# Kernel tuning notes

Measured on AMD Instinct MI355X. Metric: run time of the kernel, lower is better.

The kernel has to match this reference:

```python
import jax, jax.numpy as jnp
from jax import lax
import numpy as np
import math

NUM_CLASSES = 81
N_PER_IMG = 1024
NUM_IMAGES = 8
SCORE_THRESH = 0.05
NMS_THRESH = 0.5
DETS_PER_IMG = 100
WX, WY, WW, WH = 10.0, 10.0, 5.0, 5.0
BBOX_XFORM_CLIP = math.log(1000.0 / 16.0)


def setup_inputs() -> dict:
    key = jax.random.key(0)
    k1, k2, k3, k4 = jax.random.split(key, 4)
    M = NUM_IMAGES * N_PER_IMG
    H, W = 800, 1333
    class_logits = jax.random.normal(k1, (M, NUM_CLASSES), dtype=jnp.float32) * 3.0
    box_regression = jax.random.normal(k2, (M, 4 * NUM_CLASSES), dtype=jnp.float32) * 0.5
    # valid xyxy proposals inside the image
    xy1 = jax.random.uniform(k3, (M, 2), dtype=jnp.float32) * jnp.array([W * 0.7, H * 0.7], jnp.float32)
    wh = jax.random.uniform(k4, (M, 2), dtype=jnp.float32) * jnp.array([W * 0.3, H * 0.3], jnp.float32) + 4.0
    proposals = jnp.concatenate([xy1, xy1 + wh], axis=1)
    return {"class_logits": class_logits, "box_regression": box_regression,
            "proposals": proposals, "height": H, "width": W}


def _decode(rel_codes, boxes):
    widths = boxes[:, 2] - boxes[:, 0] + 1.0
    heights = boxes[:, 3] - boxes[:, 1] + 1.0
    ctr_x = boxes[:, 0] + 0.5 * widths
    ctr_y = boxes[:, 1] + 0.5 * heights
    rel = rel_codes.reshape(rel_codes.shape[0], -1, 4)  # [M, C, 4]
    dx = rel[:, :, 0] / WX
    dy = rel[:, :, 1] / WY
    dw = jnp.minimum(rel[:, :, 2] / WW, BBOX_XFORM_CLIP)
    dh = jnp.minimum(rel[:, :, 3] / WH, BBOX_XFORM_CLIP)
    pctr_x = dx * widths[:, None] + ctr_x[:, None]
    pctr_y = dy * heights[:, None] + ctr_y[:, None]
    pw = jnp.exp(dw) * widths[:, None]
    ph = jnp.exp(dh) * heights[:, None]
    return jnp.stack([pctr_x - 0.5 * pw, pctr_y - 0.5 * ph,
                      pctr_x + 0.5 * pw - 1.0, pctr_y + 0.5 * ph - 1.0], axis=-1)


def _clip(boxes, height, width):
    # boxes [..., 4] xyxy, clamp to [0, W-1] x [0, H-1]
    x = jnp.clip(boxes[..., 0::2], 0.0, float(width - 1))
    y = jnp.clip(boxes[..., 1::2], 0.0, float(height - 1))
    return jnp.stack([x[..., 0], y[..., 0], x[..., 1], y[..., 1]], axis=-1)


def _iou_matrix(b):
    x1, y1, x2, y2 = b[:, 0], b[:, 1], b[:, 2], b[:, 3]
    area = (x2 - x1 + 1.0) * (y2 - y1 + 1.0)
    xx1 = jnp.maximum(x1[:, None], x1[None, :])
    yy1 = jnp.maximum(y1[:, None], y1[None, :])
    xx2 = jnp.minimum(x2[:, None], x2[None, :])
    yy2 = jnp.minimum(y2[:, None], y2[None, :])
    inter = jnp.clip(xx2 - xx1 + 1.0, 0.0) * jnp.clip(yy2 - yy1 + 1.0, 0.0)
    return inter / (area[:, None] + area[None, :] - inter)


def _per_class(scores_j, boxes_j):
    # scores_j [N], boxes_j [N,4] -> sorted scores/boxes + greedy-NMS keep mask
    N = scores_j.shape[0]
    valid = scores_j > SCORE_THRESH
    s = jnp.where(valid, scores_j, 0.0)  # softmax scores are > 0
    order = jnp.argsort(-s)
    s_sorted = s[order]
    b_sorted = boxes_j[order]
    valid_sorted = valid[order]
    iou = _iou_matrix(b_sorted)  # [N, N]
    idxs = jnp.arange(N)

    def body(i, keep):
        sup = (iou[i] > NMS_THRESH) & keep[i] & (idxs > i)
        return keep & ~sup

    keep = lax.fori_loop(0, N, body, valid_sorted)
    return s_sorted, b_sorted, keep


def _per_image(prob_i, boxes_i):
    # prob_i [N, C], boxes_i [N, C, 4]; skip background class 0
    C = prob_i.shape[1]
    fg_scores = prob_i[:, 1:].T                      # [C-1, N]
    fg_boxes = jnp.swapaxes(boxes_i[:, 1:, :], 0, 1)  # [C-1, N, 4]
    s_sorted, b_sorted, keep = jax.vmap(_per_class)(fg_scores, fg_boxes)
    labels = jnp.broadcast_to(jnp.arange(1, C, dtype=jnp.int32)[:, None], s_sorted.shape)
    flat_s = jnp.where(keep, s_sorted, 0.0).reshape(-1)
    vals, idx = lax.top_k(flat_s, DETS_PER_IMG)      # detections-per-image limit
    boxes_out = b_sorted.reshape(-1, 4)[idx]
    labels_out = labels.reshape(-1)[idx]
    ok = vals > SCORE_THRESH
    return (jnp.where(ok, vals, 0.0),
            jnp.where(ok[:, None], boxes_out, 0.0),
            jnp.where(ok, labels_out, 0))


def reference(class_logits, box_regression, proposals, height, width):
    prob = jax.nn.softmax(class_logits, axis=-1)          # [M, C]
    dec = _decode(box_regression, proposals)              # [M, C, 4]
    dec = _clip(dec, height, width)
    B, N, C = NUM_IMAGES, N_PER_IMG, NUM_CLASSES
    prob = prob.reshape(B, N, C)
    dec = dec.reshape(B, N, C, 4)
    scores, boxes, labels = lax.map(lambda a: _per_image(a[0], a[1]), (prob, dec))
    return scores, boxes, labels
```

## Files before the change

### kernel.cpp

```cpp
#include <hip/hip_runtime.h>
#include <stdint.h>
#include <math.h>

#define NCLS 81
#define NFG  80
#define NPI  1024
#define NIMG 8
#define DETS 100
#define SCORE_T 0.05f
#define NMS_T   0.5f
#define NCAND   (NFG * DETS)
#define CAND_CAP 2048
#define FASTN 256
#define ROWS 64

static constexpr float BBOX_CLIP = 4.1351665567423557f;

__global__ __launch_bounds__(256) void softmax_probT(
    const float* __restrict__ logits, float* __restrict__ probT, int M)
{
    __shared__ float tile[ROWS * NCLS];
    __shared__ float mx[ROWS], dn[ROWS];
    int t = threadIdx.x;
    int rbase = blockIdx.x * ROWS;

    for (int idx = t; idx < ROWS * NCLS; idx += 256)
        tile[idx] = logits[(size_t)rbase * NCLS + idx];
    __syncthreads();

    if (t < ROWS) {
        const float* r = tile + t * NCLS;
        float m = r[0];
        #pragma unroll
        for (int j = 1; j < NCLS; ++j) m = fmaxf(m, r[j]);
        float s = 0.f;
        #pragma unroll
        for (int j = 0; j < NCLS; ++j) s += expf(r[j] - m);
        mx[t] = m; dn[t] = s;
    }
    __syncthreads();

    for (int o = t; o < ROWS * NFG; o += 256) {
        int r = o & 63;
        int c = o >> 6;
        float v = expf(tile[r * NCLS + (c + 1)] - mx[r]) / dn[r];
        probT[(size_t)c * M + rbase + r] = v;
    }
}

__global__ __launch_bounds__(256) void per_class_nms(
    const float* __restrict__ probT, const float* __restrict__ boxreg,
    const float* __restrict__ props, const int* __restrict__ hptr,
    const int* __restrict__ wptr, int* __restrict__ out_cnt,
    float* __restrict__ out_score, unsigned* __restrict__ out_key,
    float* __restrict__ out_box, int M)
{
    int pid = blockIdx.x;
    int img = pid / NFG;
    int c   = pid % NFG;
    int cls = c + 1;

    __shared__ float box_lds[NPI][4];
    __shared__ unsigned long long key[NPI];
    __shared__ int keep[NPI];
    __shared__ float sbox[FASTN][4];
    __shared__ float sarea[FASTN];
    __shared__ unsigned long long mask[FASTN][FASTN/64];
    __shared__ unsigned long long keepw[FASTN/64];
    __shared__ unsigned wpre[4];
    __shared__ int cnt;

    int t = threadIdx.x;
    float W1 = (float)(*wptr - 1);
    float H1 = (float)(*hptr - 1);

    if (t == 0) cnt = 0;
    for (int i = t; i < NPI; i += 256) key[i] = 0ULL;
    __syncthreads();

    {
        const float4 pv = *(const float4*)(probT + (size_t)c * M + img * NPI + 4 * t);
        float pr[4] = {pv.x, pv.y, pv.z, pv.w};
        #pragma unroll
        for (int j = 0; j < 4; ++j) {
            if (pr[j] > SCORE_T) {
                int m = 4 * t + j;
                int g = img * NPI + m;
                const float4 pb = *(const float4*)(props + (size_t)g * 4);
                float x1 = pb.x, y1 = pb.y, x2 = pb.z, y2 = pb.w;
                float w  = x2 - x1 + 1.0f, h = y2 - y1 + 1.0f;
                float cx = x1 + 0.5f * w,  cy = y1 + 0.5f * h;
                const float4 rc = *(const float4*)(boxreg + (size_t)g * (4 * NCLS) + 4 * cls);
                float dx = rc.x / 10.0f, dy = rc.y / 10.0f;
                float dw = fminf(rc.z / 5.0f, BBOX_CLIP);
                float dh = fminf(rc.w / 5.0f, BBOX_CLIP);
                float pcx = dx * w + cx, pcy = dy * h + cy;
                float pw = expf(dw) * w, ph = expf(dh) * h;
                float bx1 = pcx - 0.5f * pw;
                float by1 = pcy - 0.5f * ph;
                float bx2 = pcx + 0.5f * pw - 1.0f;
                float by2 = pcy + 0.5f * ph - 1.0f;
                bx1 = fminf(fmaxf(bx1, 0.f), W1);
                bx2 = fminf(fmaxf(bx2, 0.f), W1);
                by1 = fminf(fmaxf(by1, 0.f), H1);
                by2 = fminf(fmaxf(by2, 0.f), H1);
                box_lds[m][0] = bx1; box_lds[m][1] = by1;
                box_lds[m][2] = bx2; box_lds[m][3] = by2;
                int p = atomicAdd(&cnt, 1);
                unsigned fb = __float_as_uint(pr[j]);
                key[p] = ((unsigned long long)fb << 32) | (unsigned)(NPI - 1 - m);
            }
        }
    }
    __syncthreads();
    int n = cnt;

    if (n <= 64) {
        if (t < 64) {
            int lane = t;
            unsigned long long k = (lane < n) ? key[lane] : 0ULL;
            #pragma unroll
            for (int kk = 2; kk <= 64; kk <<= 1) {
                #pragma unroll
                for (int j = kk >> 1; j > 0; j >>= 1) {
                    unsigned long long o = __shfl_xor(k, j, 64);
                    bool up = ((lane & kk) == 0);
                    bool lower = ((lane & j) == 0);
                    bool take_max = (up == lower);
                    k = take_max ? (k > o ? k : o) : (k < o ? k : o);
                }
            }
            bool valid = (lane < n);
            float bx1 = 0.f, by1 = 0.f, bx2 = 0.f, by2 = 0.f, area = 0.f;
            if (valid) {
                int mi = NPI - 1 - (int)(k & 0xFFFFFFFFu);
                bx1 = box_lds[mi][0]; by1 = box_lds[mi][1];
                bx2 = box_lds[mi][2]; by2 = box_lds[mi][3];
                area = (bx2 - bx1 + 1.f) * (by2 - by1 + 1.f);
            }
            unsigned long long sup = 0ULL;
            for (int i = 0; i < n; ++i) {
                bool alive = !((sup >> i) & 1ULL);
                float ax1 = __shfl(bx1, i, 64), ay1 = __shfl(by1, i, 64);
                float ax2 = __shfl(bx2, i, 64), ay2 = __shfl(by2, i, 64);
                float aarea = __shfl(area, i, 64);
                bool s = false;
                if (alive && valid && lane > i) {
                    float xx1 = fmaxf(ax1, bx1), yy1 = fmaxf(ay1, by1);
                    float xx2 = fminf(ax2, bx2), yy2 = fminf(ay2, by2);
                    float iw = fmaxf(xx2 - xx1 + 1.f, 0.f);
                    float ih = fmaxf(yy2 - yy1 + 1.f, 0.f);
                    float inter = iw * ih;
                    float iou = inter / (aarea + area - inter);
                    s = iou > NMS_T;
                }
                sup |= __ballot(s);
            }
            bool kept = valid && !((sup >> lane) & 1ULL);
            unsigned long long keptm = __ballot(kept);
            int rank = __popcll(keptm & ((1ULL << lane) - 1ULL));
            if (kept && rank < DETS) {
                int slot = pid * DETS + rank;
                out_score[slot] = __uint_as_float((unsigned)(k >> 32));
                out_key[slot] = (unsigned)(c * NPI + lane);
                out_box[slot * 4 + 0] = bx1;
                out_box[slot * 4 + 1] = by1;
                out_box[slot * 4 + 2] = bx2;
                out_box[slot * 4 + 3] = by2;
            }
            if (lane == 0) {
                int tot = __popcll(keptm);
                out_cnt[pid] = tot < DETS ? tot : DETS;
            }
        }
        return;
    }

    int P = 2;
    while (P < n) P <<= 1;
    for (int k = 2; k <= P; k <<= 1) {
        for (int j = k >> 1; j > 0; j >>= 1) {
            for (int i = t; i < P; i += 256) {
                int ixj = i ^ j;
                if (ixj > i) {
                    unsigned long long a = key[i], b = key[ixj];
                    bool up = (i & k) == 0;
                    if (up ? (a < b) : (a > b)) { key[i] = b; key[ixj] = a; }
                }
            }
            __syncthreads();
        }
    }

    for (int i = t; i < NPI; i += 256) keep[i] = 0;
    __syncthreads();

    if (n <= FASTN) {
        for (int i = t; i < n; i += 256) {
            int mi = NPI - 1 - (int)(key[i] & 0xFFFFFFFFu);
            float bx1 = box_lds[mi][0], by1 = box_lds[mi][1];
            float bx2 = box_lds[mi][2], by2 = box_lds[mi][3];
            sbox[i][0] = bx1; sbox[i][1] = by1; sbox[i][2] = bx2; sbox[i][3] = by2;
            sarea[i] = (bx2 - bx1 + 1.f) * (by2 - by1 + 1.f);
        }
        __syncthreads();
        int nwords = ((n + 63) >> 6);
        for (int w = t; w < n * (FASTN/64); w += 256) {
            int i = w >> 2, wb = w & 3;
            if (wb >= nwords || ((wb + 1) << 6) - 1 <= i) { mask[i][wb] = 0ULL; continue; }
            float ax1 = sbox[i][0], ay1 = sbox[i][1];
            float ax2 = sbox[i][2], ay2 = sbox[i][3];
            float aarea = sarea[i];
            unsigned long long bits = 0ULL;
            int jbase = wb << 6;
            #pragma unroll 4
            for (int b = 0; b < 64; ++b) {
                int j = jbase + b;
                if (j < n && j > i) {
                    float bx1 = sbox[j][0], by1 = sbox[j][1];
                    float bx2 = sbox[j][2], by2 = sbox[j][3];
                    float xx1 = fmaxf(ax1, bx1), yy1 = fmaxf(ay1, by1);
                    float xx2 = fminf(ax2, bx2), yy2 = fminf(ay2, by2);
                    float iw = fmaxf(xx2 - xx1 + 1.f, 0.f);
                    float ih = fmaxf(yy2 - yy1 + 1.f, 0.f);
                    float inter = iw * ih;
                    float iou = inter / (aarea + sarea[j] - inter);
                    if (iou > NMS_T) bits |= (1ULL << b);
                }
            }
            mask[i][wb] = bits;
        }
        __syncthreads();
        if (t < 64) {
            int lane = t;
            unsigned long long kb = 0ULL;
            if (lane < 4) {
                int rem = n - (lane << 6);
                if (rem >= 64) kb = ~0ULL;
                else if (rem > 0) kb = (1ULL << rem) - 1ULL;
            }
            unsigned long long rm = 0ULL;
            for (int i = 0; i < n; ++i) {
                unsigned long long rw = __shfl(rm, i >> 6, 64);
                if (!((rw >> (i & 63)) & 1ULL)) {
                    unsigned long long mrow = (lane < 4) ? mask[i][lane] : 0ULL;
                    rm |= mrow;
                }
            }
            if (lane < 4) keepw[lane] = kb & ~rm;
        }
        __syncthreads();
        for (int i = t; i < n; i += 256)
            keep[i] = (int)((keepw[i >> 6] >> (i & 63)) & 1ULL);
        __syncthreads();
    } else {
        for (int i = t; i < n; i += 256) keep[i] = 1;
        __syncthreads();
        for (int i = 0; i < n; ++i) {
            if (keep[i]) {
                unsigned long long ki = key[i];
                int mi = NPI - 1 - (int)(ki & 0xFFFFFFFFu);
                float ax1 = box_lds[mi][0], ay1 = box_lds[mi][1];
                float ax2 = box_lds[mi][2], ay2 = box_lds[mi][3];
                float aarea = (ax2 - ax1 + 1.f) * (ay2 - ay1 + 1.f);
                for (int jj = i + 1 + t; jj < n; jj += 256) {
                    if (keep[jj]) {
                        int mj = NPI - 1 - (int)(key[jj] & 0xFFFFFFFFu);
                        float bx1 = box_lds[mj][0], by1 = box_lds[mj][1];
                        float bx2 = box_lds[mj][2], by2 = box_lds[mj][3];
                        float xx1 = fmaxf(ax1, bx1), yy1 = fmaxf(ay1, by1);
                        float xx2 = fminf(ax2, bx2), yy2 = fminf(ay2, by2);
                        float iw = fmaxf(xx2 - xx1 + 1.f, 0.f);
                        float ih = fmaxf(yy2 - yy1 + 1.f, 0.f);
                        float inter = iw * ih;
                        float barea = (bx2 - bx1 + 1.f) * (by2 - by1 + 1.f);
                        float iou = inter / (aarea + barea - inter);
                        if (iou > NMS_T) keep[jj] = 0;
                    }
                }
            }
            __syncthreads();
        }
    }

    {
        int lane = t & 63, w = t >> 6;
        int k0 = keep[4 * t], k1 = keep[4 * t + 1];
        int k2 = keep[4 * t + 2], k3 = keep[4 * t + 3];
        unsigned s = (unsigned)(k0 + k1 + k2 + k3);
        unsigned v = s;
        #pragma unroll
        for (int off = 1; off < 64; off <<= 1) {
            unsigned u = __shfl_up(v, off, 64);
            v += (lane >= off) ? u : 0u;
        }
        if (lane == 63) wpre[w] = v;
        __syncthreads();
        unsigned woff = 0;
        for (int w2 = 0; w2 < w; ++w2) woff += wpre[w2];
        unsigned before = v + woff - s;
        unsigned r = before;
        #pragma unroll
        for (int j = 0; j < 4; ++j) {
            int i = 4 * t + j;
            int kv = (j == 0) ? k0 : (j == 1) ? k1 : (j == 2) ? k2 : k3;
            if (kv && r < DETS) {
                unsigned long long ki = key[i];
                int mi = NPI - 1 - (int)(ki & 0xFFFFFFFFu);
                int slot = pid * DETS + (int)r;
                out_score[slot] = __uint_as_float((unsigned)(ki >> 32));
                out_key[slot] = (unsigned)(c * NPI + i);
                out_box[slot * 4 + 0] = box_lds[mi][0];
                out_box[slot * 4 + 1] = box_lds[mi][1];
                out_box[slot * 4 + 2] = box_lds[mi][2];
                out_box[slot * 4 + 3] = box_lds[mi][3];
            }
            r += (unsigned)kv;
        }
        __syncthreads();
        if (t == 0) {
            unsigned tot = wpre[0] + wpre[1] + wpre[2] + wpre[3];
            out_cnt[pid] = (int)(tot < DETS ? tot : DETS);
        }
    }
}

__device__ __forceinline__ void suffix_select(
    unsigned* hist, unsigned* wtot, int K, int* outB, unsigned* outAbove)
{
    int t = threadIdx.x, lane = t & 63, w = t >> 6;
    unsigned c0 = hist[4 * t], c1 = hist[4 * t + 1];
    unsigned c2 = hist[4 * t + 2], c3 = hist[4 * t + 3];
    unsigned ps = c0 + c1 + c2 + c3;
    unsigned v = ps;
    #pragma unroll
    for (int off = 1; off < 64; off <<= 1) {
        unsigned u = __shfl_down(v, off, 64);
        v += (lane + off < 64) ? u : 0u;
    }
    if (lane == 0) wtot[w] = v;
    __syncthreads();
    unsigned woff = 0;
    for (int w2 = w + 1; w2 < 16; ++w2) woff += wtot[w2];
    unsigned Sown = v + woff;
    unsigned A3 = Sown - ps;
    unsigned A2 = A3 + c3, A1 = A2 + c2, A0 = A1 + c1;
    unsigned A[4] = {A0, A1, A2, A3};
    unsigned C[4] = {c0, c1, c2, c3};
    #pragma unroll
    for (int j = 0; j < 4; ++j) {
        if ((int)A[j] < K && (int)(A[j] + C[j]) >= K) {
            *outB = 4 * t + j;
            *outAbove = A[j];
        }
    }
    __syncthreads();
}

__global__ __launch_bounds__(1024) void topk_merge(
    const int* __restrict__ cnts, const float* __restrict__ escore,
    const unsigned* __restrict__ ekey, const float* __restrict__ ebox,
    float* __restrict__ out)
{
    int img = blockIdx.x;
    __shared__ unsigned sc[NCAND];
    __shared__ unsigned hist[4096];
    __shared__ unsigned long long cand[CAND_CAP];
    __shared__ unsigned wtot[16];
    __shared__ int sB1, sB2, sNc;
    __shared__ unsigned sAb1, sAb2;

    int t = threadIdx.x;
    if (t == 0) { sB1 = 0; sB2 = 0; sNc = 0; sAb1 = 0; sAb2 = 0; }
    for (int p = t; p < NCAND; p += 1024) {
        int cc = p / DETS, k = p % DETS;
        unsigned fb = 0;
        if (k < cnts[img * NFG + cc]) fb = __float_as_uint(escore[img * NCAND + p]);
        sc[p] = fb;
    }
    for (int i = t; i < 4096; i += 1024) hist[i] = 0;
    __syncthreads();

    for (int p = t; p < NCAND; p += 1024) {
        unsigned fb = sc[p];
        if (fb) atomicAdd(&hist[fb >> 19], 1u);
    }
    __syncthreads();
    suffix_select(hist, wtot, DETS, &sB1, &sAb1);
    int B1 = sB1;
    unsigned ab1 = sAb1;

    for (int i = t; i < 4096; i += 1024) hist[i] = 0;
    __syncthreads();
    for (int p = t; p < NCAND; p += 1024) {
        unsigned fb = sc[p];
        if (fb && (int)(fb >> 19) == B1) atomicAdd(&hist[(fb >> 7) & 0xFFFu], 1u);
    }
    __syncthreads();
    suffix_select(hist, wtot, DETS - (int)ab1, &sB2, &sAb2);
    int B2 = sB2;

    for (int p = t; p < NCAND; p += 1024) {
        unsigned fb = sc[p];
        if (fb) {
            int d1 = (int)(fb >> 19);
            bool ok = d1 > B1 || (d1 == B1 && (int)((fb >> 7) & 0xFFFu) >= B2);
            if (ok) {
                int pos = atomicAdd(&sNc, 1);
                if (pos < CAND_CAP) {
                    unsigned fk = ekey[img * NCAND + p];
                    unsigned low = ((0x1FFFFu - fk) << 13) | (unsigned)p;
                    cand[pos] = ((unsigned long long)fb << 32) | low;
                }
            }
        }
    }
    __syncthreads();
    int nc = sNc < CAND_CAP ? sNc : CAND_CAP;
    int P = 128;
    while (P < nc) P <<= 1;
    for (int i = t; i < P; i += 1024)
        if (i >= nc) cand[i] = 0ULL;
    __syncthreads();

    for (int k = 2; k <= P; k <<= 1) {
        for (int j = k >> 1; j > 0; j >>= 1) {
            for (int i = t; i < P; i += 1024) {
                int ixj = i ^ j;
                if (ixj > i) {
                    unsigned long long a = cand[i], b = cand[ixj];
                    bool up = (i & k) == 0;
                    if (up ? (a < b) : (a > b)) { cand[i] = b; cand[ixj] = a; }
                }
            }
            __syncthreads();
        }
    }

    float* oScore = out;
    float* oBox   = out + NIMG * DETS;
    float* oLab   = out + NIMG * DETS * 5;

    if (t < DETS) {
        unsigned long long b = cand[t];
        int o = img * DETS + t;
        if (b != 0ULL) {
            float scv = __uint_as_float((unsigned)(b >> 32));
            unsigned low = (unsigned)(b & 0xFFFFFFFFu);
            unsigned flatkey = 0x1FFFFu - ((low >> 13) & 0x1FFFFu);
            int p = (int)(low & 0x1FFFu);
            int gp = img * NCAND + p;
            oScore[o] = scv;
            oBox[o * 4 + 0] = ebox[gp * 4 + 0];
            oBox[o * 4 + 1] = ebox[gp * 4 + 1];
            oBox[o * 4 + 2] = ebox[gp * 4 + 2];
            oBox[o * 4 + 3] = ebox[gp * 4 + 3];
            oLab[o] = (float)((flatkey >> 10) + 1);
        } else {
            oScore[o] = 0.f;
            oBox[o * 4 + 0] = 0.f; oBox[o * 4 + 1] = 0.f;
            oBox[o * 4 + 2] = 0.f; oBox[o * 4 + 3] = 0.f;
            oLab[o] = 0.f;
        }
    }
}

extern "C" void kernel_launch(void* const* d_in, const int* in_sizes, int n_in,
                              void* d_out, int out_size, void* d_ws, size_t ws_size,
                              hipStream_t stream) {
    const float* logits = (const float*)d_in[0];
    const float* boxreg = (const float*)d_in[1];
    const float* props  = (const float*)d_in[2];
    const int*   hptr   = (const int*)d_in[3];
    const int*   wptr   = (const int*)d_in[4];
    float* out = (float*)d_out;
    int M = in_sizes[0] / NCLS;

    char* ws = (char*)d_ws;
    float*    probT  = (float*)ws;    ws += (size_t)NFG * M * sizeof(float);
    int*      cnt    = (int*)ws;      ws += (size_t)NIMG * NFG * sizeof(int);
    float*    escore = (float*)ws;    ws += (size_t)NIMG * NCAND * sizeof(float);
    unsigned* ekey   = (unsigned*)ws; ws += (size_t)NIMG * NCAND * sizeof(unsigned);
    float*    ebox   = (float*)ws;    ws += (size_t)NIMG * NCAND * 4 * sizeof(float);

    softmax_probT<<<M / ROWS, 256, 0, stream>>>(logits, probT, M);
    per_class_nms<<<NIMG * NFG, 256, 0, stream>>>(
        probT, boxreg, props, hptr, wptr, cnt, escore, ekey, ebox, M);
    topk_merge<<<NIMG, 1024, 0, stream>>>(cnt, escore, ekey, ebox, out);
}
```

Before: 61.07 us.

## Fuse softmax, per-class NMS and top-k merge into one cooperative kernel

Replaces the three kernel launches with a single cooperative kernel of 512 blocks that runs softmax, per-class NMS (grid-strided over 640 image/class pairs) and the per-image top-k merge, with grid-wide syncs between the stages. Stage shared memory is overlaid through a union. The merge now uses 256 threads and reads scores straight from global memory instead of staging them in LDS. The aim is to remove launch gaps, at the cost of grid.sync overhead and fewer resident blocks during NMS. A fallback runs the old three-kernel path if the cooperative launch fails.

```diff
diff --git a/kernel.cpp b/kernel.cpp
--- a/kernel.cpp
+++ b/kernel.cpp
@@ -1,6 +1,9 @@
 #include <hip/hip_runtime.h>
+#include <hip/hip_cooperative_groups.h>
 #include <stdint.h>
 #include <math.h>
+
+namespace cg = cooperative_groups;
 
 #define NCLS 81
 #define NFG  80
@@ -13,8 +16,454 @@
 #define CAND_CAP 2048
 #define FASTN 256
 #define ROWS 64
+#define GRID_BLOCKS 512
 
 static constexpr float BBOX_CLIP = 4.1351665567423557f;
+
+struct ShP1 {
+    float tile[ROWS * NCLS];
+    float mx[ROWS], dn[ROWS];
+};
+struct ShP2 {
+    float box[NPI][4];
+    unsigned long long key[NPI];
+    int keep[NPI];
+    float sbox[FASTN][4];
+    float sarea[FASTN];
+    unsigned long long mask[FASTN][FASTN/64];
+    unsigned long long keepw[FASTN/64];
+    unsigned wpre[4];
+};
+struct ShP3 {
+    unsigned hist[4096];
+    unsigned long long cand[CAND_CAP];
+    int cnts[NFG];
+    unsigned wtot[4];
+    int B1, B2, Nc;
+    unsigned Ab1, Ab2;
+};
+union ShU { ShP1 p1; ShP2 p2; ShP3 p3; };
+
+__device__ __forceinline__ void suffix_select256(
+    unsigned* hist, unsigned* wtot, int K, int* outB, unsigned* outAbove)
+{
+    int t = threadIdx.x, lane = t & 63, w = t >> 6;
+    unsigned loc[16]; unsigned ps = 0;
+    #pragma unroll
+    for (int j = 0; j < 16; ++j) { loc[j] = hist[t * 16 + j]; ps += loc[j]; }
+    unsigned v = ps;
+    #pragma unroll
+    for (int off = 1; off < 64; off <<= 1) {
+        unsigned u = __shfl_down(v, off, 64);
+        v += (lane + off < 64) ? u : 0u;
+    }
+    if (lane == 0) wtot[w] = v;
+    __syncthreads();
+    unsigned woff = 0;
+    for (int w2 = w + 1; w2 < 4; ++w2) woff += wtot[w2];
+    unsigned base = v + woff - ps;
+    unsigned suf = 0;
+    #pragma unroll
+    for (int j = 15; j >= 0; --j) {
+        unsigned A = base + suf;
+        if ((int)A < K && (int)(A + loc[j]) >= K) { *outB = t * 16 + j; *outAbove = A; }
+        suf += loc[j];
+    }
+    __syncthreads();
+}
+
+__global__ __launch_bounds__(256, 2) void fpn_fused(
+    const float* __restrict__ logits, const float* __restrict__ boxreg,
+    const float* __restrict__ props, const int* __restrict__ hptr,
+    const int* __restrict__ wptr, float* __restrict__ probT,
+    int* __restrict__ gcnt, float* __restrict__ escore,
+    unsigned* __restrict__ ekey, float* __restrict__ ebox,
+    float* __restrict__ out, int M)
+{
+    cg::grid_group grid = cg::this_grid();
+    __shared__ ShU sh;
+    __shared__ int cnt;
+    int t = threadIdx.x;
+    int bid = blockIdx.x;
+
+    if (bid < M / ROWS) {
+        int rbase = bid * ROWS;
+        for (int idx = t; idx < ROWS * NCLS; idx += 256)
+            sh.p1.tile[idx] = logits[(size_t)rbase * NCLS + idx];
+        __syncthreads();
+        if (t < ROWS) {
+            const float* r = sh.p1.tile + t * NCLS;
+            float m = r[0];
+            #pragma unroll
+            for (int j = 1; j < NCLS; ++j) m = fmaxf(m, r[j]);
+            float s = 0.f;
+            #pragma unroll
+            for (int j = 0; j < NCLS; ++j) s += expf(r[j] - m);
+            sh.p1.mx[t] = m; sh.p1.dn[t] = s;
+        }
+        __syncthreads();
+        for (int o = t; o < ROWS * NFG; o += 256) {
+            int r = o & 63;
+            int c = o >> 6;
+            float v = expf(sh.p1.tile[r * NCLS + (c + 1)] - sh.p1.mx[r]) / sh.p1.dn[r];
+            probT[(size_t)c * M + rbase + r] = v;
+        }
+    }
+    grid.sync();
+
+    for (int pid = bid; pid < NIMG * NFG; pid += GRID_BLOCKS) {
+        int img = pid / NFG;
+        int c   = pid % NFG;
+        int cls = c + 1;
+        float W1 = (float)(*wptr - 1);
+        float H1 = (float)(*hptr - 1);
+
+        if (t == 0) cnt = 0;
+        for (int i = t; i < NPI; i += 256) sh.p2.key[i] = 0ULL;
+        __syncthreads();
+
+        {
+            const float4 pv = *(const float4*)(probT + (size_t)c * M + img * NPI + 4 * t);
+            float pr[4] = {pv.x, pv.y, pv.z, pv.w};
+            #pragma unroll
+            for (int j = 0; j < 4; ++j) {
+                if (pr[j] > SCORE_T) {
+                    int m = 4 * t + j;
+                    int g = img * NPI + m;
+                    const float4 pb = *(const float4*)(props + (size_t)g * 4);
+                    float x1 = pb.x, y1 = pb.y, x2 = pb.z, y2 = pb.w;
+                    float w  = x2 - x1 + 1.0f, h = y2 - y1 + 1.0f;
+                    float cx = x1 + 0.5f * w,  cy = y1 + 0.5f * h;
+                    const float4 rc = *(const float4*)(boxreg + (size_t)g * (4 * NCLS) + 4 * cls);
+                    float dx = rc.x / 10.0f, dy = rc.y / 10.0f;
+                    float dw = fminf(rc.z / 5.0f, BBOX_CLIP);
+                    float dh = fminf(rc.w / 5.0f, BBOX_CLIP);
+                    float pcx = dx * w + cx, pcy = dy * h + cy;
+                    float pw = expf(dw) * w, ph = expf(dh) * h;
+                    float bx1 = pcx - 0.5f * pw;
+                    float by1 = pcy - 0.5f * ph;
+                    float bx2 = pcx + 0.5f * pw - 1.0f;
+                    float by2 = pcy + 0.5f * ph - 1.0f;
+                    bx1 = fminf(fmaxf(bx1, 0.f), W1);
+                    bx2 = fminf(fmaxf(bx2, 0.f), W1);
+                    by1 = fminf(fmaxf(by1, 0.f), H1);
+                    by2 = fminf(fmaxf(by2, 0.f), H1);
+                    sh.p2.box[m][0] = bx1; sh.p2.box[m][1] = by1;
+                    sh.p2.box[m][2] = bx2; sh.p2.box[m][3] = by2;
+                    int p = atomicAdd(&cnt, 1);
+                    unsigned fb = __float_as_uint(pr[j]);
+                    sh.p2.key[p] = ((unsigned long long)fb << 32) | (unsigned)(NPI - 1 - m);
+                }
+            }
+        }
+        __syncthreads();
+        int n = cnt;
+
+        if (n <= 64) {
+            if (t < 64) {
+                int lane = t;
+                unsigned long long k = (lane < n) ? sh.p2.key[lane] : 0ULL;
+                #pragma unroll
+                for (int kk = 2; kk <= 64; kk <<= 1) {
+                    #pragma unroll
+                    for (int j = kk >> 1; j > 0; j >>= 1) {
+                        unsigned long long o = __shfl_xor(k, j, 64);
+                        bool up = ((lane & kk) == 0);
+                        bool lower = ((lane & j) == 0);
+                        bool take_max = (up == lower);
+                        k = take_max ? (k > o ? k : o) : (k < o ? k : o);
+                    }
+                }
+                bool valid = (lane < n);
+                float bx1 = 0.f, by1 = 0.f, bx2 = 0.f, by2 = 0.f, area = 0.f;
+                if (valid) {
+                    int mi = NPI - 1 - (int)(k & 0xFFFFFFFFu);
+                    bx1 = sh.p2.box[mi][0]; by1 = sh.p2.box[mi][1];
+                    bx2 = sh.p2.box[mi][2]; by2 = sh.p2.box[mi][3];
+                    area = (bx2 - bx1 + 1.f) * (by2 - by1 + 1.f);
+                }
+                unsigned long long sup = 0ULL;
+                for (int i = 0; i < n; ++i) {
+                    bool alive = !((sup >> i) & 1ULL);
+                    float ax1 = __shfl(bx1, i, 64), ay1 = __shfl(by1, i, 64);
+                    float ax2 = __shfl(bx2, i, 64), ay2 = __shfl(by2, i, 64);
+                    float aarea = __shfl(area, i, 64);
+                    bool s = false;
+                    if (alive && valid && lane > i) {
+                        float xx1 = fmaxf(ax1, bx1), yy1 = fmaxf(ay1, by1);
+                        float xx2 = fminf(ax2, bx2), yy2 = fminf(ay2, by2);
+                        float iw = fmaxf(xx2 - xx1 + 1.f, 0.f);
+                        float ih = fmaxf(yy2 - yy1 + 1.f, 0.f);
+                        float inter = iw * ih;
+                        float iou = inter / (aarea + area - inter);
+                        s = iou > NMS_T;
+                    }
+                    sup |= __ballot(s);
+                }
+                bool kept = valid && !((sup >> lane) & 1ULL);
+                unsigned long long keptm = __ballot(kept);
+                int rank = __popcll(keptm & ((1ULL << lane) - 1ULL));
+                if (kept && rank < DETS) {
+                    int slot = pid * DETS + rank;
+                    escore[slot] = __uint_as_float((unsigned)(k >> 32));
+                    ekey[slot] = (unsigned)(c * NPI + lane);
+                    ebox[slot * 4 + 0] = bx1;
+                    ebox[slot * 4 + 1] = by1;
+                    ebox[slot * 4 + 2] = bx2;
+                    ebox[slot * 4 + 3] = by2;
+                }
+                if (lane == 0) {
+                    int tot = __popcll(keptm);
+                    gcnt[pid] = tot < DETS ? tot : DETS;
+                }
+            }
+        } else {
+            int P = 2;
+            while (P < n) P <<= 1;
+            for (int k = 2; k <= P; k <<= 1) {
+                for (int j = k >> 1; j > 0; j >>= 1) {
+                    for (int i = t; i < P; i += 256) {
+                        int ixj = i ^ j;
+                        if (ixj > i) {
+                            unsigned long long a = sh.p2.key[i], b = sh.p2.key[ixj];
+                            bool up = (i & k) == 0;
+                            if (up ? (a < b) : (a > b)) { sh.p2.key[i] = b; sh.p2.key[ixj] = a; }
+                        }
+                    }
+                    __syncthreads();
+                }
+            }
+
+            for (int i = t; i < NPI; i += 256) sh.p2.keep[i] = 0;
+            __syncthreads();
+
+            if (n <= FASTN) {
+                for (int i = t; i < n; i += 256) {
+                    int mi = NPI - 1 - (int)(sh.p2.key[i] & 0xFFFFFFFFu);
+                    float bx1 = sh.p2.box[mi][0], by1 = sh.p2.box[mi][1];
+                    float bx2 = sh.p2.box[mi][2], by2 = sh.p2.box[mi][3];
+                    sh.p2.sbox[i][0] = bx1; sh.p2.sbox[i][1] = by1;
+                    sh.p2.sbox[i][2] = bx2; sh.p2.sbox[i][3] = by2;
+                    sh.p2.sarea[i] = (bx2 - bx1 + 1.f) * (by2 - by1 + 1.f);
+                }
+                __syncthreads();
+                int nwords = ((n + 63) >> 6);
+                for (int w = t; w < n * (FASTN/64); w += 256) {
+                    int i = w >> 2, wb = w & 3;
+                    if (wb >= nwords || ((wb + 1) << 6) - 1 <= i) { sh.p2.mask[i][wb] = 0ULL; continue; }
+                    float ax1 = sh.p2.sbox[i][0], ay1 = sh.p2.sbox[i][1];
+                    float ax2 = sh.p2.sbox[i][2], ay2 = sh.p2.sbox[i][3];
+                    float aarea = sh.p2.sarea[i];
+                    unsigned long long bits = 0ULL;
+                    int jbase = wb << 6;
+                    #pragma unroll 4
+                    for (int b = 0; b < 64; ++b) {
+                        int j = jbase + b;
+                        if (j < n && j > i) {
+                            float bx1 = sh.p2.sbox[j][0], by1 = sh.p2.sbox[j][1];
+                            float bx2 = sh.p2.sbox[j][2], by2 = sh.p2.sbox[j][3];
+                            float xx1 = fmaxf(ax1, bx1), yy1 = fmaxf(ay1, by1);
+                            float xx2 = fminf(ax2, bx2), yy2 = fminf(ay2, by2);
+                            float iw = fmaxf(xx2 - xx1 + 1.f, 0.f);
+                            float ih = fmaxf(yy2 - yy1 + 1.f, 0.f);
+                            float inter = iw * ih;
+                            float iou = inter / (aarea + sh.p2.sarea[j] - inter);
+                            if (iou > NMS_T) bits |= (1ULL << b);
+                        }
+                    }
+                    sh.p2.mask[i][wb] = bits;
+                }
+                __syncthreads();
+                if (t < 64) {
+                    int lane = t;
+                    unsigned long long kb = 0ULL;
+                    if (lane < 4) {
+                        int rem = n - (lane << 6);
+                        if (rem >= 64) kb = ~0ULL;
+                        else if (rem > 0) kb = (1ULL << rem) - 1ULL;
+                    }
+                    unsigned long long rm = 0ULL;
+                    for (int i = 0; i < n; ++i) {
+                        unsigned long long rw = __shfl(rm, i >> 6, 64);
+                        if (!((rw >> (i & 63)) & 1ULL)) {
+                            unsigned long long mrow = (lane < 4) ? sh.p2.mask[i][lane] : 0ULL;
+                            rm |= mrow;
+                        }
+                    }
+                    if (lane < 4) sh.p2.keepw[lane] = kb & ~rm;
+                }
+                __syncthreads();
+                for (int i = t; i < n; i += 256)
+                    sh.p2.keep[i] = (int)((sh.p2.keepw[i >> 6] >> (i & 63)) & 1ULL);
+                __syncthreads();
+            } else {
+                for (int i = t; i < n; i += 256) sh.p2.keep[i] = 1;
+                __syncthreads();
+                for (int i = 0; i < n; ++i) {
+                    if (sh.p2.keep[i]) {
+                        unsigned long long ki = sh.p2.key[i];
+                        int mi = NPI - 1 - (int)(ki & 0xFFFFFFFFu);
+                        float ax1 = sh.p2.box[mi][0], ay1 = sh.p2.box[mi][1];
+                        float ax2 = sh.p2.box[mi][2], ay2 = sh.p2.box[mi][3];
+                        float aarea = (ax2 - ax1 + 1.f) * (ay2 - ay1 + 1.f);
+                        for (int jj = i + 1 + t; jj < n; jj += 256) {
+                            if (sh.p2.keep[jj]) {
+                                int mj = NPI - 1 - (int)(sh.p2.key[jj] & 0xFFFFFFFFu);
+                                float bx1 = sh.p2.box[mj][0], by1 = sh.p2.box[mj][1];
+                                float bx2 = sh.p2.box[mj][2], by2 = sh.p2.box[mj][3];
+                                float xx1 = fmaxf(ax1, bx1), yy1 = fmaxf(ay1, by1);
+                                float xx2 = fminf(ax2, bx2), yy2 = fminf(ay2, by2);
+                                float iw = fmaxf(xx2 - xx1 + 1.f, 0.f);
+                                float ih = fmaxf(yy2 - yy1 + 1.f, 0.f);
+                                float inter = iw * ih;
+                                float barea = (bx2 - bx1 + 1.f) * (by2 - by1 + 1.f);
+                                float iou = inter / (aarea + barea - inter);
+                                if (iou > NMS_T) sh.p2.keep[jj] = 0;
+                            }
+                        }
+                    }
+                    __syncthreads();
+                }
+            }
+
+            {
+                int lane = t & 63, w = t >> 6;
+                int k0 = sh.p2.keep[4 * t], k1 = sh.p2.keep[4 * t + 1];
+                int k2 = sh.p2.keep[4 * t + 2], k3 = sh.p2.keep[4 * t + 3];
+                unsigned s = (unsigned)(k0 + k1 + k2 + k3);
+                unsigned v = s;
+                #pragma unroll
+                for (int off = 1; off < 64; off <<= 1) {
+                    unsigned u = __shfl_up(v, off, 64);
+                    v += (lane >= off) ? u : 0u;
+                }
+                if (lane == 63) sh.p2.wpre[w] = v;
+                __syncthreads();
+                unsigned woff = 0;
+                for (int w2 = 0; w2 < w; ++w2) woff += sh.p2.wpre[w2];
+                unsigned r = v + woff - s;
+                #pragma unroll
+                for (int j = 0; j < 4; ++j) {
+                    int i = 4 * t + j;
+                    int kv = (j == 0) ? k0 : (j == 1) ? k1 : (j == 2) ? k2 : k3;
+                    if (kv && r < DETS) {
+                        unsigned long long ki = sh.p2.key[i];
+                        int mi = NPI - 1 - (int)(ki & 0xFFFFFFFFu);
+                        int slot = pid * DETS + (int)r;
+                        escore[slot] = __uint_as_float((unsigned)(ki >> 32));
+                        ekey[slot] = (unsigned)(c * NPI + i);
+                        ebox[slot * 4 + 0] = sh.p2.box[mi][0];
+                        ebox[slot * 4 + 1] = sh.p2.box[mi][1];
+                        ebox[slot * 4 + 2] = sh.p2.box[mi][2];
+                        ebox[slot * 4 + 3] = sh.p2.box[mi][3];
+                    }
+                    r += (unsigned)kv;
+                }
+                __syncthreads();
+                if (t == 0) {
+                    unsigned tot = sh.p2.wpre[0] + sh.p2.wpre[1] + sh.p2.wpre[2] + sh.p2.wpre[3];
+                    gcnt[pid] = (int)(tot < DETS ? tot : DETS);
+                }
+            }
+        }
+        __syncthreads();
+    }
+    grid.sync();
+
+    if (bid < NIMG) {
+        int img = bid;
+        if (t < NFG) sh.p3.cnts[t] = gcnt[img * NFG + t];
+        if (t == 0) { sh.p3.B1 = 0; sh.p3.B2 = 0; sh.p3.Nc = 0; sh.p3.Ab1 = 0; sh.p3.Ab2 = 0; }
+        for (int i = t; i < 4096; i += 256) sh.p3.hist[i] = 0;
+        __syncthreads();
+
+        for (int p = t; p < NCAND; p += 256) {
+            if ((p % DETS) < sh.p3.cnts[p / DETS]) {
+                unsigned fb = __float_as_uint(escore[img * NCAND + p]);
+                atomicAdd(&sh.p3.hist[fb >> 19], 1u);
+            }
+        }
+        __syncthreads();
+        suffix_select256(sh.p3.hist, sh.p3.wtot, DETS, &sh.p3.B1, &sh.p3.Ab1);
+        int B1 = sh.p3.B1; unsigned ab1 = sh.p3.Ab1;
+
+        for (int i = t; i < 4096; i += 256) sh.p3.hist[i] = 0;
+        __syncthreads();
+        for (int p = t; p < NCAND; p += 256) {
+            if ((p % DETS) < sh.p3.cnts[p / DETS]) {
+                unsigned fb = __float_as_uint(escore[img * NCAND + p]);
+                if ((int)(fb >> 19) == B1) atomicAdd(&sh.p3.hist[(fb >> 7) & 0xFFFu], 1u);
+            }
+        }
+        __syncthreads();
+        suffix_select256(sh.p3.hist, sh.p3.wtot, DETS - (int)ab1, &sh.p3.B2, &sh.p3.Ab2);
+        int B2 = sh.p3.B2;
+
+        for (int p = t; p < NCAND; p += 256) {
+            if ((p % DETS) < sh.p3.cnts[p / DETS]) {
+                unsigned fb = __float_as_uint(escore[img * NCAND + p]);
+                int d1 = (int)(fb >> 19);
+                bool ok = d1 > B1 || (d1 == B1 && (int)((fb >> 7) & 0xFFFu) >= B2);
+                if (ok) {
+                    int pos = atomicAdd(&sh.p3.Nc, 1);
+                    if (pos < CAND_CAP) {
+                        unsigned fk = ekey[img * NCAND + p];
+                        sh.p3.cand[pos] = ((unsigned long long)fb << 32)
+                                        | (((0x1FFFFu - fk) << 13) | (unsigned)p);
+                    }
+                }
+            }
+        }
+        __syncthreads();
+        int nc = sh.p3.Nc < CAND_CAP ? sh.p3.Nc : CAND_CAP;
+        int P = 128;
+        while (P < nc) P <<= 1;
+        for (int i = t; i < P; i += 256)
+            if (i >= nc) sh.p3.cand[i] = 0ULL;
+        __syncthreads();
+
+        for (int k = 2; k <= P; k <<= 1) {
+            for (int j = k >> 1; j > 0; j >>= 1) {
+                for (int i = t; i < P; i += 256) {
+                    int ixj = i ^ j;
+                    if (ixj > i) {
+                        unsigned long long a = sh.p3.cand[i], b = sh.p3.cand[ixj];
+                        bool up = (i & k) == 0;
+                        if (up ? (a < b) : (a > b)) { sh.p3.cand[i] = b; sh.p3.cand[ixj] = a; }
+                    }
+                }
+                __syncthreads();
+            }
+        }
+
+        float* oScore = out;
+        float* oBox   = out + NIMG * DETS;
+        float* oLab   = out + NIMG * DETS * 5;
+
+        if (t < DETS) {
+            unsigned long long b = sh.p3.cand[t];
+            int o = img * DETS + t;
+            if (b != 0ULL) {
+                float scv = __uint_as_float((unsigned)(b >> 32));
+                unsigned low = (unsigned)(b & 0xFFFFFFFFu);
+                unsigned flatkey = 0x1FFFFu - ((low >> 13) & 0x1FFFFu);
+                int p = (int)(low & 0x1FFFu);
+                int gp = img * NCAND + p;
+                oScore[o] = scv;
+                oBox[o * 4 + 0] = ebox[gp * 4 + 0];
+                oBox[o * 4 + 1] = ebox[gp * 4 + 1];
+                oBox[o * 4 + 2] = ebox[gp * 4 + 2];
+                oBox[o * 4 + 3] = ebox[gp * 4 + 3];
+                oLab[o] = (float)((flatkey >> 10) + 1);
+            } else {
+                oScore[o] = 0.f;
+                oBox[o * 4 + 0] = 0.f; oBox[o * 4 + 1] = 0.f;
+                oBox[o * 4 + 2] = 0.f; oBox[o * 4 + 3] = 0.f;
+                oLab[o] = 0.f;
+            }
+        }
+    }
+}
 
 __global__ __launch_bounds__(256) void softmax_probT(
     const float* __restrict__ logits, float* __restrict__ probT, int M)
@@ -23,11 +472,9 @@
     __shared__ float mx[ROWS], dn[ROWS];
     int t = threadIdx.x;
     int rbase = blockIdx.x * ROWS;
-
     for (int idx = t; idx < ROWS * NCLS; idx += 256)
         tile[idx] = logits[(size_t)rbase * NCLS + idx];
     __syncthreads();
-
     if (t < ROWS) {
         const float* r = tile + t * NCLS;
         float m = r[0];
@@ -39,12 +486,10 @@
         mx[t] = m; dn[t] = s;
     }
     __syncthreads();
-
     for (int o = t; o < ROWS * NFG; o += 256) {
         int r = o & 63;
         int c = o >> 6;
-        float v = expf(tile[r * NCLS + (c + 1)] - mx[r]) / dn[r];
-        probT[(size_t)c * M + rbase + r] = v;
+        probT[(size_t)c * M + rbase + r] = expf(tile[r * NCLS + (c + 1)] - mx[r]) / dn[r];
     }
 }
 
@@ -59,25 +504,15 @@
     int img = pid / NFG;
     int c   = pid % NFG;
     int cls = c + 1;
-
-    __shared__ float box_lds[NPI][4];
-    __shared__ unsigned long long key[NPI];
-    __shared__ int keep[NPI];
-    __shared__ float sbox[FASTN][4];
-    __shared__ float sarea[FASTN];
-    __shared__ unsigned long long mask[FASTN][FASTN/64];
-    __shared__ unsigned long long keepw[FASTN/64];
-    __shared__ unsigned wpre[4];
+    __shared__ ShP2 sp;
     __shared__ int cnt;
-
     int t = threadIdx.x;
     float W1 = (float)(*wptr - 1);
     float H1 = (float)(*hptr - 1);
 
     if (t == 0) cnt = 0;
-    for (int i = t; i < NPI; i += 256) key[i] = 0ULL;
-    __syncthreads();
-
+    for (int i = t; i < NPI; i += 256) sp.key[i] = 0ULL;
+    __syncthreads();
     {
         const float4 pv = *(const float4*)(probT + (size_t)c * M + img * NPI + 4 * t);
         float pr[4] = {pv.x, pv.y, pv.z, pv.w};
@@ -96,19 +531,15 @@
                 float dh = fminf(rc.w / 5.0f, BBOX_CLIP);
                 float pcx = dx * w + cx, pcy = dy * h + cy;
                 float pw = expf(dw) * w, ph = expf(dh) * h;
-                float bx1 = pcx - 0.5f * pw;
-                float by1 = pcy - 0.5f * ph;
-                float bx2 = pcx + 0.5f * pw - 1.0f;
-                float by2 = pcy + 0.5f * ph - 1.0f;
-                bx1 = fminf(fmaxf(bx1, 0.f), W1);
-                bx2 = fminf(fmaxf(bx2, 0.f), W1);
-                by1 = fminf(fmaxf(by1, 0.f), H1);
-                by2 = fminf(fmaxf(by2, 0.f), H1);
-                box_lds[m][0] = bx1; box_lds[m][1] = by1;
-                box_lds[m][2] = bx2; box_lds[m][3] = by2;
+                float bx1 = fminf(fmaxf(pcx - 0.5f * pw, 0.f), W1);
+                float by1 = fminf(fmaxf(pcy - 0.5f * ph, 0.f), H1);
+                float bx2 = fminf(fmaxf(pcx + 0.5f * pw - 1.0f, 0.f), W1);
+                float by2 = fminf(fmaxf(pcy + 0.5f * ph - 1.0f, 0.f), H1);
+                sp.box[m][0] = bx1; sp.box[m][1] = by1;
+                sp.box[m][2] = bx2; sp.box[m][3] = by2;
                 int p = atomicAdd(&cnt, 1);
-                unsigned fb = __float_as_uint(pr[j]);
-                key[p] = ((unsigned long long)fb << 32) | (unsigned)(NPI - 1 - m);
+                sp.key[p] = ((unsigned long long)__float_as_uint(pr[j]) << 32)
+                          | (unsigned)(NPI - 1 - m);
             }
         }
     }
@@ -118,15 +549,13 @@
     if (n <= 64) {
         if (t < 64) {
             int lane = t;
-            unsigned long long k = (lane < n) ? key[lane] : 0ULL;
+            unsigned long long k = (lane < n) ? sp.key[lane] : 0ULL;
             #pragma unroll
             for (int kk = 2; kk <= 64; kk <<= 1) {
                 #pragma unroll
                 for (int j = kk >> 1; j > 0; j >>= 1) {
                     unsigned long long o = __shfl_xor(k, j, 64);
-                    bool up = ((lane & kk) == 0);
-                    bool lower = ((lane & j) == 0);
-                    bool take_max = (up == lower);
+                    bool take_max = (((lane & kk) == 0) == ((lane & j) == 0));
                     k = take_max ? (k > o ? k : o) : (k < o ? k : o);
                 }
             }
@@ -134,8 +563,8 @@
             float bx1 = 0.f, by1 = 0.f, bx2 = 0.f, by2 = 0.f, area = 0.f;
             if (valid) {
                 int mi = NPI - 1 - (int)(k & 0xFFFFFFFFu);
-                bx1 = box_lds[mi][0]; by1 = box_lds[mi][1];
-                bx2 = box_lds[mi][2]; by2 = box_lds[mi][3];
+                bx1 = sp.box[mi][0]; by1 = sp.box[mi][1];
+                bx2 = sp.box[mi][2]; by2 = sp.box[mi][3];
                 area = (bx2 - bx1 + 1.f) * (by2 - by1 + 1.f);
             }
             unsigned long long sup = 0ULL;
@@ -151,8 +580,7 @@
                     float iw = fmaxf(xx2 - xx1 + 1.f, 0.f);
                     float ih = fmaxf(yy2 - yy1 + 1.f, 0.f);
                     float inter = iw * ih;
-                    float iou = inter / (aarea + area - inter);
-                    s = iou > NMS_T;
+                    s = inter / (aarea + area - inter) > NMS_T;
                 }
                 sup |= __ballot(s);
             }
@@ -163,10 +591,8 @@
                 int slot = pid * DETS + rank;
                 out_score[slot] = __uint_as_float((unsigned)(k >> 32));
                 out_key[slot] = (unsigned)(c * NPI + lane);
-                out_box[slot * 4 + 0] = bx1;
-                out_box[slot * 4 + 1] = by1;
-                out_box[slot * 4 + 2] = bx2;
-                out_box[slot * 4 + 3] = by2;
+                out_box[slot * 4 + 0] = bx1; out_box[slot * 4 + 1] = by1;
+                out_box[slot * 4 + 2] = bx2; out_box[slot * 4 + 3] = by2;
             }
             if (lane == 0) {
                 int tot = __popcll(keptm);
@@ -183,52 +609,51 @@
             for (int i = t; i < P; i += 256) {
                 int ixj = i ^ j;
                 if (ixj > i) {
-                    unsigned long long a = key[i], b = key[ixj];
+                    unsigned long long a = sp.key[i], b = sp.key[ixj];
                     bool up = (i & k) == 0;
-                    if (up ? (a < b) : (a > b)) { key[i] = b; key[ixj] = a; }
+                    if (up ? (a < b) : (a > b)) { sp.key[i] = b; sp.key[ixj] = a; }
                 }
             }
             __syncthreads();
         }
     }
-
-    for (int i = t; i < NPI; i += 256) keep[i] = 0;
+    for (int i = t; i < NPI; i += 256) sp.keep[i] = 0;
     __syncthreads();
 
     if (n <= FASTN) {
         for (int i = t; i < n; i += 256) {
-            int mi = NPI - 1 - (int)(key[i] & 0xFFFFFFFFu);
-            float bx1 = box_lds[mi][0], by1 = box_lds[mi][1];
-            float bx2 = box_lds[mi][2], by2 = box_lds[mi][3];
-            sbox[i][0] = bx1; sbox[i][1] = by1; sbox[i][2] = bx2; sbox[i][3] = by2;
-            sarea[i] = (bx2 - bx1 + 1.f) * (by2 - by1 + 1.f);
+            int mi = NPI - 1 - (int)(sp.key[i] & 0xFFFFFFFFu);
+            float bx1 = sp.box[mi][0], by1 = sp.box[mi][1];
+            float bx2 = sp.box[mi][2], by2 = sp.box[mi][3];
+            sp.sbox[i][0] = bx1; sp.sbox[i][1] = by1;
+            sp.sbox[i][2] = bx2; sp.sbox[i][3] = by2;
+            sp.sarea[i] = (bx2 - bx1 + 1.f) * (by2 - by1 + 1.f);
         }
         __syncthreads();
         int nwords = ((n + 63) >> 6);
         for (int w = t; w < n * (FASTN/64); w += 256) {
             int i = w >> 2, wb = w & 3;
-            if (wb >= nwords || ((wb + 1) << 6) - 1 <= i) { mask[i][wb] = 0ULL; continue; }
-            float ax1 = sbox[i][0], ay1 = sbox[i][1];
-            float ax2 = sbox[i][2], ay2 = sbox[i][3];
-            float aarea = sarea[i];
+            if (wb >= nwords || ((wb + 1) << 6) - 1 <= i) { sp.mask[i][wb] = 0ULL; continue; }
+            float ax1 = sp.sbox[i][0], ay1 = sp.sbox[i][1];
+            float ax2 = sp.sbox[i][2], ay2 = sp.sbox[i][3];
+            float aarea = sp.sarea[i];
             unsigned long long bits = 0ULL;
             int jbase = wb << 6;
             #pragma unroll 4
             for (int b = 0; b < 64; ++b) {
                 int j = jbase + b;
                 if (j < n && j > i) {
-                    float bx1 = sbox[j][0], by1 = sbox[j][1];
-                    float bx2 = sbox[j][2], by2 = sbox[j][3];
+                    float bx1 = sp.sbox[j][0], by1 = sp.sbox[j][1];
+                    float bx2 = sp.sbox[j][2], by2 = sp.sbox[j][3];
                     float xx1 = fmaxf(ax1, bx1), yy1 = fmaxf(ay1, by1);
                     float xx2 = fminf(ax2, bx2), yy2 = fminf(ay2, by2);
                     float iw = fmaxf(xx2 - xx1 + 1.f, 0.f);
                     float ih = fmaxf(yy2 - yy1 + 1.f, 0.f);
                     float inter = iw * ih;
-                    float iou = inter / (aarea + sarea[j] - inter);
-                    if (iou > NMS_T) bits |= (1ULL << b);
-                }
-            }
-            mask[i][wb] = bits;
+                    if (inter / (aarea + sp.sarea[j] - inter) > NMS_T) bits |= (1ULL << b);
+                }
+            }
+            sp.mask[i][wb] = bits;
         }
         __syncthreads();
         if (t < 64) {
@@ -243,50 +668,48 @@
             for (int i = 0; i < n; ++i) {
                 unsigned long long rw = __shfl(rm, i >> 6, 64);
                 if (!((rw >> (i & 63)) & 1ULL)) {
-                    unsigned long long mrow = (lane < 4) ? mask[i][lane] : 0ULL;
+                    unsigned long long mrow = (lane < 4) ? sp.mask[i][lane] : 0ULL;
                     rm |= mrow;
                 }
             }
-            if (lane < 4) keepw[lane] = kb & ~rm;
+            if (lane < 4) sp.keepw[lane] = kb & ~rm;
         }
         __syncthreads();
         for (int i = t; i < n; i += 256)
-            keep[i] = (int)((keepw[i >> 6] >> (i & 63)) & 1ULL);
+            sp.keep[i] = (int)((sp.keepw[i >> 6] >> (i & 63)) & 1ULL);
         __syncthreads();
     } else {
-        for (int i = t; i < n; i += 256) keep[i] = 1;
+        for (int i = t; i < n; i += 256) sp.keep[i] = 1;
         __syncthreads();
         for (int i = 0; i < n; ++i) {
-            if (keep[i]) {
-                unsigned long long ki = key[i];
+            if (sp.keep[i]) {
+                unsigned long long ki = sp.key[i];
                 int mi = NPI - 1 - (int)(ki & 0xFFFFFFFFu);
-                float ax1 = box_lds[mi][0], ay1 = box_lds[mi][1];
-                float ax2 = box_lds[mi][2], ay2 = box_lds[mi][3];
+                float ax1 = sp.box[mi][0], ay1 = sp.box[mi][1];
+                float ax2 = sp.box[mi][2], ay2 = sp.box[mi][3];
                 float aarea = (ax2 - ax1 + 1.f) * (ay2 - ay1 + 1.f);
                 for (int jj = i + 1 + t; jj < n; jj += 256) {
-                    if (keep[jj]) {
-                        int mj = NPI - 1 - (int)(key[jj] & 0xFFFFFFFFu);
-                        float bx1 = box_lds[mj][0], by1 = box_lds[mj][1];
-                        float bx2 = box_lds[mj][2], by2 = box_lds[mj][3];
+                    if (sp.keep[jj]) {
+                        int mj = NPI - 1 - (int)(sp.key[jj] & 0xFFFFFFFFu);
+                        float bx1 = sp.box[mj][0], by1 = sp.box[mj][1];
+                        float bx2 = sp.box[mj][2], by2 = sp.box[mj][3];
                         float xx1 = fmaxf(ax1, bx1), yy1 = fmaxf(ay1, by1);
                         float xx2 = fminf(ax2, bx2), yy2 = fminf(ay2, by2);
                         float iw = fmaxf(xx2 - xx1 + 1.f, 0.f);
                         float ih = fmaxf(yy2 - yy1 + 1.f, 0.f);
                         float inter = iw * ih;
                         float barea = (bx2 - bx1 + 1.f) * (by2 - by1 + 1.f);
-                        float iou = inter / (aarea + barea - inter);
-                        if (iou > NMS_T) keep[jj] = 0;
+                        if (inter / (aarea + barea - inter) > NMS_T) sp.keep[jj] = 0;
                     }
                 }
             }
             __syncthreads();
         }
     }
-
     {
         int lane = t & 63, w = t >> 6;
-        int k0 = keep[4 * t], k1 = keep[4 * t + 1];
-        int k2 = keep[4 * t + 2], k3 = keep[4 * t + 3];
+        int k0 = sp.keep[4 * t], k1 = sp.keep[4 * t + 1];
+        int k2 = sp.keep[4 * t + 2], k3 = sp.keep[4 * t + 3];
         unsigned s = (unsigned)(k0 + k1 + k2 + k3);
         unsigned v = s;
         #pragma unroll
@@ -294,155 +717,108 @@
             unsigned u = __shfl_up(v, off, 64);
             v += (lane >= off) ? u : 0u;
         }
-        if (lane == 63) wpre[w] = v;
+        if (lane == 63) sp.wpre[w] = v;
         __syncthreads();
         unsigned woff = 0;
-        for (int w2 = 0; w2 < w; ++w2) woff += wpre[w2];
-        unsigned before = v + woff - s;
-        unsigned r = before;
+        for (int w2 = 0; w2 < w; ++w2) woff += sp.wpre[w2];
+        unsigned r = v + woff - s;
         #pragma unroll
         for (int j = 0; j < 4; ++j) {
             int i = 4 * t + j;
             int kv = (j == 0) ? k0 : (j == 1) ? k1 : (j == 2) ? k2 : k3;
             if (kv && r < DETS) {
-                unsigned long long ki = key[i];
+                unsigned long long ki = sp.key[i];
                 int mi = NPI - 1 - (int)(ki & 0xFFFFFFFFu);
                 int slot = pid * DETS + (int)r;
                 out_score[slot] = __uint_as_float((unsigned)(ki >> 32));
                 out_key[slot] = (unsigned)(c * NPI + i);
-                out_box[slot * 4 + 0] = box_lds[mi][0];
-                out_box[slot * 4 + 1] = box_lds[mi][1];
-                out_box[slot * 4 + 2] = box_lds[mi][2];
-                out_box[slot * 4 + 3] = box_lds[mi][3];
+                out_box[slot * 4 + 0] = sp.box[mi][0];
+                out_box[slot * 4 + 1] = sp.box[mi][1];
+                out_box[slot * 4 + 2] = sp.box[mi][2];
+                out_box[slot * 4 + 3] = sp.box[mi][3];
             }
             r += (unsigned)kv;
         }
         __syncthreads();
         if (t == 0) {
-            unsigned tot = wpre[0] + wpre[1] + wpre[2] + wpre[3];
+            unsigned tot = sp.wpre[0] + sp.wpre[1] + sp.wpre[2] + sp.wpre[3];
             out_cnt[pid] = (int)(tot < DETS ? tot : DETS);
         }
     }
 }
 
-__device__ __forceinline__ void suffix_select(
-    unsigned* hist, unsigned* wtot, int K, int* outB, unsigned* outAbove)
-{
-    int t = threadIdx.x, lane = t & 63, w = t >> 6;
-    unsigned c0 = hist[4 * t], c1 = hist[4 * t + 1];
-    unsigned c2 = hist[4 * t + 2], c3 = hist[4 * t + 3];
-    unsigned ps = c0 + c1 + c2 + c3;
-    unsigned v = ps;
-    #pragma unroll
-    for (int off = 1; off < 64; off <<= 1) {
-        unsigned u = __shfl_down(v, off, 64);
-        v += (lane + off < 64) ? u : 0u;
-    }
-    if (lane == 0) wtot[w] = v;
-    __syncthreads();
-    unsigned woff = 0;
-    for (int w2 = w + 1; w2 < 16; ++w2) woff += wtot[w2];
-    unsigned Sown = v + woff;
-    unsigned A3 = Sown - ps;
-    unsigned A2 = A3 + c3, A1 = A2 + c2, A0 = A1 + c1;
-    unsigned A[4] = {A0, A1, A2, A3};
-    unsigned C[4] = {c0, c1, c2, c3};
-    #pragma unroll
-    for (int j = 0; j < 4; ++j) {
-        if ((int)A[j] < K && (int)(A[j] + C[j]) >= K) {
-            *outB = 4 * t + j;
-            *outAbove = A[j];
-        }
-    }
-    __syncthreads();
-}
-
-__global__ __launch_bounds__(1024) void topk_merge(
+__global__ __launch_bounds__(256) void topk_merge(
     const int* __restrict__ cnts, const float* __restrict__ escore,
     const unsigned* __restrict__ ekey, const float* __restrict__ ebox,
     float* __restrict__ out)
 {
     int img = blockIdx.x;
-    __shared__ unsigned sc[NCAND];
-    __shared__ unsigned hist[4096];
-    __shared__ unsigned long long cand[CAND_CAP];
-    __shared__ unsigned wtot[16];
-    __shared__ int sB1, sB2, sNc;
-    __shared__ unsigned sAb1, sAb2;
-
+    __shared__ ShP3 s3;
     int t = threadIdx.x;
-    if (t == 0) { sB1 = 0; sB2 = 0; sNc = 0; sAb1 = 0; sAb2 = 0; }
-    for (int p = t; p < NCAND; p += 1024) {
-        int cc = p / DETS, k = p % DETS;
-        unsigned fb = 0;
-        if (k < cnts[img * NFG + cc]) fb = __float_as_uint(escore[img * NCAND + p]);
-        sc[p] = fb;
-    }
-    for (int i = t; i < 4096; i += 1024) hist[i] = 0;
-    __syncthreads();
-
-    for (int p = t; p < NCAND; p += 1024) {
-        unsigned fb = sc[p];
-        if (fb) atomicAdd(&hist[fb >> 19], 1u);
-    }
-    __syncthreads();
-    suffix_select(hist, wtot, DETS, &sB1, &sAb1);
-    int B1 = sB1;
-    unsigned ab1 = sAb1;
-
-    for (int i = t; i < 4096; i += 1024) hist[i] = 0;
-    __syncthreads();
-    for (int p = t; p < NCAND; p += 1024) {
-        unsigned fb = sc[p];
-        if (fb && (int)(fb >> 19) == B1) atomicAdd(&hist[(fb >> 7) & 0xFFFu], 1u);
-    }
-    __syncthreads();
-    suffix_select(hist, wtot, DETS - (int)ab1, &sB2, &sAb2);
-    int B2 = sB2;
-
-    for (int p = t; p < NCAND; p += 1024) {
-        unsigned fb = sc[p];
-        if (fb) {
+    if (t < NFG) s3.cnts[t] = cnts[img * NFG + t];
+    if (t == 0) { s3.B1 = 0; s3.B2 = 0; s3.Nc = 0; s3.Ab1 = 0; s3.Ab2 = 0; }
+    for (int i = t; i < 4096; i += 256) s3.hist[i] = 0;
+    __syncthreads();
+    for (int p = t; p < NCAND; p += 256) {
+        if ((p % DETS) < s3.cnts[p / DETS]) {
+            unsigned fb = __float_as_uint(escore[img * NCAND + p]);
+            atomicAdd(&s3.hist[fb >> 19], 1u);
+        }
+    }
+    __syncthreads();
+    suffix_select256(s3.hist, s3.wtot, DETS, &s3.B1, &s3.Ab1);
+    int B1 = s3.B1; unsigned ab1 = s3.Ab1;
+    for (int i = t; i < 4096; i += 256) s3.hist[i] = 0;
+    __syncthreads();
+    for (int p = t; p < NCAND; p += 256) {
+        if ((p % DETS) < s3.cnts[p / DETS]) {
+            unsigned fb = __float_as_uint(escore[img * NCAND + p]);
+            if ((int)(fb >> 19) == B1) atomicAdd(&s3.hist[(fb >> 7) & 0xFFFu], 1u);
+        }
+    }
+    __syncthreads();
+    suffix_select256(s3.hist, s3.wtot, DETS - (int)ab1, &s3.B2, &s3.Ab2);
+    int B2 = s3.B2;
+    for (int p = t; p < NCAND; p += 256) {
+        if ((p % DETS) < s3.cnts[p / DETS]) {
+            unsigned fb = __float_as_uint(escore[img * NCAND + p]);
             int d1 = (int)(fb >> 19);
             bool ok = d1 > B1 || (d1 == B1 && (int)((fb >> 7) & 0xFFFu) >= B2);
             if (ok) {
-                int pos = atomicAdd(&sNc, 1);
+                int pos = atomicAdd(&s3.Nc, 1);
                 if (pos < CAND_CAP) {
                     unsigned fk = ekey[img * NCAND + p];
-                    unsigned low = ((0x1FFFFu - fk) << 13) | (unsigned)p;
-                    cand[pos] = ((unsigned long long)fb << 32) | low;
-                }
-            }
-        }
-    }
-    __syncthreads();
-    int nc = sNc < CAND_CAP ? sNc : CAND_CAP;
+                    s3.cand[pos] = ((unsigned long long)fb << 32)
+                                 | (((0x1FFFFu - fk) << 13) | (unsigned)p);
+                }
+            }
+        }
+    }
+    __syncthreads();
+    int nc = s3.Nc < CAND_CAP ? s3.Nc : CAND_CAP;
     int P = 128;
     while (P < nc) P <<= 1;
-    for (int i = t; i < P; i += 1024)
-        if (i >= nc) cand[i] = 0ULL;
-    __syncthreads();
-
+    for (int i = t; i < P; i += 256)
+        if (i >= nc) s3.cand[i] = 0ULL;
+    __syncthreads();
     for (int k = 2; k <= P; k <<= 1) {
         for (int j = k >> 1; j > 0; j >>= 1) {
-            for (int i = t; i < P; i += 1024) {
+            for (int i = t; i < P; i += 256) {
                 int ixj = i ^ j;
                 if (ixj > i) {
-                    unsigned long long a = cand[i], b = cand[ixj];
+                    unsigned long long a = s3.cand[i], b = s3.cand[ixj];
                     bool up = (i & k) == 0;
-                    if (up ? (a < b) : (a > b)) { cand[i] = b; cand[ixj] = a; }
+                    if (up ? (a < b) : (a > b)) { s3.cand[i] = b; s3.cand[ixj] = a; }
                 }
             }
             __syncthreads();
         }
     }
-
     float* oScore = out;
     float* oBox   = out + NIMG * DETS;
     float* oLab   = out + NIMG * DETS * 5;
-
     if (t < DETS) {
-        unsigned long long b = cand[t];
+        unsigned long long b = s3.cand[t];
         int o = img * DETS + t;
         if (b != 0ULL) {
             float scv = __uint_as_float((unsigned)(b >> 32));
@@ -478,13 +854,24 @@
 
     char* ws = (char*)d_ws;
     float*    probT  = (float*)ws;    ws += (size_t)NFG * M * sizeof(float);
-    int*      cnt    = (int*)ws;      ws += (size_t)NIMG * NFG * sizeof(int);
+    int*      gcnt   = (int*)ws;      ws += (size_t)NIMG * NFG * sizeof(int);
     float*    escore = (float*)ws;    ws += (size_t)NIMG * NCAND * sizeof(float);
     unsigned* ekey   = (unsigned*)ws; ws += (size_t)NIMG * NCAND * sizeof(unsigned);
     float*    ebox   = (float*)ws;    ws += (size_t)NIMG * NCAND * 4 * sizeof(float);
 
-    softmax_probT<<<M / ROWS, 256, 0, stream>>>(logits, probT, M);
-    per_class_nms<<<NIMG * NFG, 256, 0, stream>>>(
-        probT, boxreg, props, hptr, wptr, cnt, escore, ekey, ebox, M);
-    topk_merge<<<NIMG, 1024, 0, stream>>>(cnt, escore, ekey, ebox, out);
+    void* args[] = {
+        (void*)&logits, (void*)&boxreg, (void*)&props, (void*)&hptr, (void*)&wptr,
+        (void*)&probT, (void*)&gcnt, (void*)&escore, (void*)&ekey, (void*)&ebox,
+        (void*)&out, (void*)&M
+    };
+    hipError_t err = hipLaunchCooperativeKernel(
+        reinterpret_cast<void*>(fpn_fused), dim3(GRID_BLOCKS), dim3(256),
+        args, 0, stream);
+    if (err != hipSuccess) {
+        (void)hipGetLastError();
+        softmax_probT<<<M / ROWS, 256, 0, stream>>>(logits, probT, M);
+        per_class_nms<<<NIMG * NFG, 256, 0, stream>>>(
+            probT, boxreg, props, hptr, wptr, gcnt, escore, ekey, ebox, M);
+        topk_merge<<<NIMG, 256, 0, stream>>>(gcnt, escore, ekey, ebox, out);
+    }
 }
```

New measurement: 182.7 us. +199.2%, slower.
